# Kernel optimization log

Measured on AMD Instinct MI355X. Metric: run time of the kernel, lower is better.

Reference implementation:

```python
import jax, jax.numpy as jnp
import numpy as np

D_MODEL = 512
N_HEADS = 8
DEPTH = D_MODEL // N_HEADS
NEG_INF = -1000000000.0


def setup_inputs() -> dict:
    key = jax.random.key(0)
    ks = jax.random.split(key, 12)
    B, S = 4, 2048
    scale = 0.02
    return {
        "Q": jax.random.normal(ks[0], (B, S, D_MODEL), jnp.float32),
        "K": jax.random.normal(ks[1], (B, S, D_MODEL), jnp.float32),
        "V": jax.random.normal(ks[2], (B, S, D_MODEL), jnp.float32),
        "mask": jax.random.randint(ks[3], (B, S, S), 0, 2, jnp.int32),
        "Wq": jax.random.normal(ks[4], (D_MODEL, D_MODEL), jnp.float32) * scale,
        "bq": jnp.zeros((D_MODEL,), jnp.float32),
        "Wk": jax.random.normal(ks[5], (D_MODEL, D_MODEL), jnp.float32) * scale,
        "bk": jnp.zeros((D_MODEL,), jnp.float32),
        "Wv": jax.random.normal(ks[6], (D_MODEL, D_MODEL), jnp.float32) * scale,
        "bv": jnp.zeros((D_MODEL,), jnp.float32),
        "Wo": jax.random.normal(ks[7], (D_MODEL, D_MODEL), jnp.float32) * scale,
        "bo": jnp.zeros((D_MODEL,), jnp.float32),
    }


def _split_heads(x, B):
    # [B, S, d_model] -> [B, H, S, depth]
    S = x.shape[1]
    return x.reshape(B, S, N_HEADS, DEPTH).transpose(0, 2, 1, 3)


def reference(Q, K, V, mask, Wq, bq, Wk, bk, Wv, bv, Wo, bo):
    B, S, _ = Q.shape
    q = _split_heads(Q @ Wq + bq, B)  # [B,H,S,d]
    k = _split_heads(K @ Wk + bk, B)
    v = _split_heads(V @ Wv + bv, B)
    scores = jnp.einsum("bhqd,bhkd->bhqk", q, k) / jnp.sqrt(
        jnp.asarray(DEPTH, jnp.float32))
    m = mask[:, None, :, :]  # broadcast over heads: [B,1,S,S]
    scores = jnp.where(m == 0, jnp.asarray(NEG_INF, scores.dtype), scores)
    attn = jax.nn.softmax(scores, axis=-1)
    ctx = jnp.einsum("bhqk,bhkd->bhqd", attn, v)
    ctx = ctx.transpose(0, 2, 1, 3).reshape(B, S, D_MODEL)
    return ctx @ Wo + bo
```

## Files before the change

kernel.cpp:

```cpp
#include <hip/hip_runtime.h>
#include <hip/hip_bf16.h>
#include <stdint.h>

typedef unsigned short u16;
typedef unsigned int u32;
typedef unsigned long long u64;
using bf16x8 = __attribute__((ext_vector_type(8))) __bf16;
using f32x4  = __attribute__((ext_vector_type(4))) float;
using f32x16 = __attribute__((ext_vector_type(16))) float;

static constexpr int B_ = 4, H_ = 8, S_ = 2048, D_ = 64, DM_ = 512;
#define QSCALE 0.1803368801111601f

__device__ __forceinline__ u16 f2b(float f) {
  u32 u = __float_as_uint(f);
  u = (u + 0x7FFFu + ((u >> 16) & 1u)) >> 16;
  return (u16)u;
}

__device__ __forceinline__ u32 cvtpk_bf16(float a, float b) {
  u32 r;
  asm("v_cvt_pk_bf16_f32 %0, %1, %2" : "=v"(r) : "v"(a), "v"(b));
  return r;
}
__device__ __forceinline__ void plswap(u32& a, u32& b) {
  asm("v_permlane32_swap_b32 %0, %1" : "+v"(a), "+v"(b));
}
__device__ __forceinline__ void gload16(const void* g, void* lds) {
  __builtin_amdgcn_global_load_lds(
      (const __attribute__((address_space(1))) u32*)g,
      (__attribute__((address_space(3))) u32*)lds, 16, 0, 0);
}
#if __has_builtin(__builtin_amdgcn_exp2f)
__device__ __forceinline__ float exp2fast(float x) { return __builtin_amdgcn_exp2f(x); }
#else
__device__ __forceinline__ float exp2fast(float x) {
  float r;
  asm("v_exp_f32 %0, %1" : "=v"(r) : "v"(x));
  return r;
}
#endif
__device__ __forceinline__ float selmask(float ex, u64 pred) {
  float r;
  asm("v_cndmask_b32 %0, 0, %1, %2" : "=v"(r) : "v"(ex), "s"(pred));
  return r;
}

__global__ __launch_bounds__(256) void prep_w_kernel(
    const float* __restrict__ Wq, const float* __restrict__ Wk,
    const float* __restrict__ Wv, const float* __restrict__ Wo,
    u16* __restrict__ Wtq, u16* __restrict__ Wtk, u16* __restrict__ Wtv, u16* __restrict__ Wto) {
  __shared__ float tile[32][33];
  const int z = blockIdx.z;
  const float* W = z == 0 ? Wq : z == 1 ? Wk : z == 2 ? Wv : Wo;
  u16* Wt       = z == 0 ? Wtq : z == 1 ? Wtk : z == 2 ? Wtv : Wto;
  const int k0 = blockIdx.x * 32, n0 = blockIdx.y * 32;
  const int t = threadIdx.x;
  {
    const int kl = t >> 3, nl4 = (t & 7) * 4;
    float4 v = *(const float4*)(W + (size_t)(k0 + kl) * DM_ + n0 + nl4);
    tile[kl][nl4 + 0] = v.x; tile[kl][nl4 + 1] = v.y;
    tile[kl][nl4 + 2] = v.z; tile[kl][nl4 + 3] = v.w;
  }
  __syncthreads();
  {
    const int nl = t >> 3, kl4 = (t & 7) * 4;
    ushort4 o;
    o.x = f2b(tile[kl4 + 0][nl]); o.y = f2b(tile[kl4 + 1][nl]);
    o.z = f2b(tile[kl4 + 2][nl]); o.w = f2b(tile[kl4 + 3][nl]);
    *(ushort4*)(Wt + (size_t)(n0 + nl) * DM_ + k0 + kl4) = o;
  }
}

__global__ __launch_bounds__(256) void pack_mask_kernel(const int* __restrict__ mask,
                                                        u64* __restrict__ wmask) {
  __shared__ int mt[4][32][65];
  const int t = threadIdx.x, lane = t & 63, w = t >> 6;
  const int kt = blockIdx.x * 4 + w, qg = blockIdx.y, b = blockIdx.z;
  const int q0 = qg * 32;
  const int* src = mask + ((size_t)b * S_ + q0) * S_ + kt * 64 + lane;
#pragma unroll 8
  for (int i = 0; i < 32; ++i) mt[w][i][lane] = src[(size_t)i * S_];
  u64* dst = wmask + (((size_t)(b * 64 + qg) * 32 + kt) * 32);
  const int hi4 = (lane >> 5) * 4;
#pragma unroll
  for (int idx = 0; idx < 32; ++idx) {
    const int ksub = idx >> 4, r = idx & 15;
    const int key = ksub * 32 + (r & 3) + 8 * (r >> 2) + hi4;
    u64 bal = __ballot(mt[w][lane & 31][key] != 0);
    if (lane == 0) dst[idx] = bal;
  }
}

__global__ __launch_bounds__(256) void gemm_qkv_kernel(
    const float* __restrict__ Qf, const float* __restrict__ Kf, const float* __restrict__ Vf,
    const u16* __restrict__ Wtq, const u16* __restrict__ Wtk, const u16* __restrict__ Wtv,
    const float* __restrict__ bq, const float* __restrict__ bk, const float* __restrict__ bv,
    u16* __restrict__ qp, u16* __restrict__ kp, u16* __restrict__ vp) {
  __shared__ u16 As[128][40];
  __shared__ u16 Bs[128][40];
  const int z = blockIdx.z;
  const float* A    = z == 0 ? Qf : z == 1 ? Kf : Vf;
  const u16* Bt     = z == 0 ? Wtq : z == 1 ? Wtk : Wtv;
  const float* bias = z == 0 ? bq : z == 1 ? bk : bv;
  u16* outp         = z == 0 ? qp : z == 1 ? kp : vp;
  const float scale = z == 0 ? QSCALE : 1.0f;

  const int t = threadIdx.x;
  const int lane = t & 63, wid = t >> 6;
  const int wr = wid >> 1, wc = wid & 1;
  const int l15 = lane & 15, l4 = lane >> 4;
  const int cn = blockIdx.x * 128, rm = blockIdx.y * 128;
  const int srow = t >> 2, scol = (t & 3) << 3;

  f32x4 acc[4][4] = {};

  for (int k0 = 0; k0 < DM_; k0 += 32) {
    __syncthreads();
    {
      const float* a0 = A + (size_t)(rm + srow) * DM_ + k0 + scol;
      float4 f0 = *(const float4*)a0, f1 = *(const float4*)(a0 + 4);
      uint4 u;
      u.x = cvtpk_bf16(f0.x, f0.y); u.y = cvtpk_bf16(f0.z, f0.w);
      u.z = cvtpk_bf16(f1.x, f1.y); u.w = cvtpk_bf16(f1.z, f1.w);
      *(uint4*)(&As[srow][scol]) = u;
      const float* a1 = A + (size_t)(rm + srow + 64) * DM_ + k0 + scol;
      float4 g0 = *(const float4*)a1, g1 = *(const float4*)(a1 + 4);
      uint4 w2;
      w2.x = cvtpk_bf16(g0.x, g0.y); w2.y = cvtpk_bf16(g0.z, g0.w);
      w2.z = cvtpk_bf16(g1.x, g1.y); w2.w = cvtpk_bf16(g1.z, g1.w);
      *(uint4*)(&As[srow + 64][scol]) = w2;
    }
    *(uint4*)(&Bs[srow][scol])      = *(const uint4*)(Bt + (size_t)(cn + srow) * DM_ + k0 + scol);
    *(uint4*)(&Bs[srow + 64][scol]) = *(const uint4*)(Bt + (size_t)(cn + srow + 64) * DM_ + k0 + scol);
    __syncthreads();
    bf16x8 af[4], bfr[4];
#pragma unroll
    for (int m = 0; m < 4; ++m)
      af[m] = *(const bf16x8*)(&As[wr * 64 + m * 16 + l15][l4 * 8]);
#pragma unroll
    for (int n = 0; n < 4; ++n)
      bfr[n] = *(const bf16x8*)(&Bs[wc * 64 + n * 16 + l15][l4 * 8]);
#pragma unroll
    for (int m = 0; m < 4; ++m)
#pragma unroll
      for (int n = 0; n < 4; ++n)
        acc[m][n] = __builtin_amdgcn_mfma_f32_16x16x32_bf16(af[m], bfr[n], acc[m][n], 0, 0, 0);
  }

#pragma unroll
  for (int m = 0; m < 4; ++m)
#pragma unroll
    for (int n = 0; n < 4; ++n) {
      int col = cn + wc * 64 + n * 16 + l15;
      float bv_ = bias[col];
#pragma unroll
      for (int r = 0; r < 4; ++r) {
        int row = rm + wr * 64 + m * 16 + l4 * 4 + r;
        float v = (acc[m][n][r] + bv_) * scale;
        int b = row >> 11, s = row & 2047;
        int h = col >> 6, d = col & 63;
        if (z < 2)
          outp[(((size_t)(b * H_ + h)) * S_ + s) * D_ + d] = f2b(v);
        else
          outp[(((size_t)(b * H_ + h)) * D_ + d) * S_ + s] = f2b(v);
      }
    }
}

__global__ __launch_bounds__(256) void gemm_out_kernel(
    const u16* __restrict__ A, const u16* __restrict__ Bt,
    const float* __restrict__ bias, float* __restrict__ outp) {
  __shared__ u16 As[64][40];
  __shared__ u16 Bs[128][40];
  const int t = threadIdx.x;
  const int lane = t & 63, w = t >> 6;
  const int l15 = lane & 15, l4 = lane >> 4;
  const int cn = blockIdx.x * 128, rm = blockIdx.y * 64;
  const int srow = t >> 2, scol = (t & 3) << 3;

  f32x4 acc[4][2] = {};

  for (int k0 = 0; k0 < DM_; k0 += 32) {
    __syncthreads();
    *(uint4*)(&As[srow][scol])      = *(const uint4*)(A + (size_t)(rm + srow) * DM_ + k0 + scol);
    *(uint4*)(&Bs[srow][scol])      = *(const uint4*)(Bt + (size_t)(cn + srow) * DM_ + k0 + scol);
    *(uint4*)(&Bs[srow + 64][scol]) = *(const uint4*)(Bt + (size_t)(cn + srow + 64) * DM_ + k0 + scol);
    __syncthreads();
    bf16x8 af[4], bfr[2];
#pragma unroll
    for (int m = 0; m < 4; ++m)
      af[m] = *(const bf16x8*)(&As[m * 16 + l15][l4 * 8]);
#pragma unroll
    for (int n = 0; n < 2; ++n)
      bfr[n] = *(const bf16x8*)(&Bs[w * 32 + n * 16 + l15][l4 * 8]);
#pragma unroll
    for (int m = 0; m < 4; ++m)
#pragma unroll
      for (int n = 0; n < 2; ++n)
        acc[m][n] = __builtin_amdgcn_mfma_f32_16x16x32_bf16(af[m], bfr[n], acc[m][n], 0, 0, 0);
  }

#pragma unroll
  for (int m = 0; m < 4; ++m)
#pragma unroll
    for (int n = 0; n < 2; ++n) {
      int col = cn + w * 32 + n * 16 + l15;
      float bv_ = bias[col];
#pragma unroll
      for (int r = 0; r < 4; ++r) {
        int row = rm + m * 16 + l4 * 4 + r;
        outp[(size_t)row * DM_ + col] = acc[m][n][r] + bv_;
      }
    }
}

__global__ __launch_bounds__(256, 4) void attn_kernel(
    const u16* __restrict__ qp, const u16* __restrict__ kp, const u16* __restrict__ vp,
    const u64* __restrict__ wmask, u16* __restrict__ ctx) {
  __shared__ __align__(16) char smem[32768];
  const int t = threadIdx.x, lane = t & 63, w = t >> 6;
  const int l31 = lane & 31, hi = lane >> 5;
  const int ksub = w & 1, qsub = w >> 1;
  const int wu = __builtin_amdgcn_readfirstlane(w);
  const int wgid = blockIdx.x;
  const int h = wgid & 7, idx = wgid >> 3;
  const int b = idx >> 5, qt = idx & 31;
  const size_t head  = ((size_t)(b * H_ + h)) * S_ * D_;
  const size_t headT = ((size_t)(b * H_ + h)) * D_ * S_;
  const int q0 = qt * 64 + qsub * 32;
  const int q  = q0 + l31;

  bf16x8 qf[4];
  {
    const u16* qrow = qp + head + (size_t)q * D_;
#pragma unroll
    for (int ks = 0; ks < 4; ++ks) qf[ks] = *(const bf16x8*)(qrow + ks * 16 + hi * 8);
  }

  const u64* wm = wmask + (((size_t)(b * 64 + qt * 2 + (wu >> 1)) * 32) * 32) + (wu & 1) * 16;

  const int kxor = (l31 & 7) << 4;
  const int krbase = (ksub * 32 + l31) * 128;
  const int rbase0 = l31 * 128, rbase1 = (32 + l31) * 128;
  int colx[4];
#pragma unroll
  for (int s = 0; s < 4; ++s) colx[s] = ((s * 32 + hi * 16) ^ kxor);
  int vcolx[2];
#pragma unroll
  for (int s = 0; s < 2; ++s) vcolx[s] = ((ksub * 64 + s * 32 + hi * 16) ^ kxor);

  const int srow = lane >> 3;
  const int scol = ((lane & 7) ^ srow) << 3;
  const int c0 = w, c1 = w + 4;
  const u16* ksrc0 = kp + head + (size_t)(c0 * 8 + srow) * D_ + scol;
  const u16* ksrc1 = kp + head + (size_t)(c1 * 8 + srow) * D_ + scol;
  const u16* vsrc0 = vp + headT + (size_t)(c0 * 8 + srow) * S_ + scol;
  const u16* vsrc1 = vp + headT + (size_t)(c1 * 8 + srow) * S_ + scol;

  f32x16 accO0, accO1, lacc, FZ;
#pragma unroll
  for (int i = 0; i < 16; ++i) { accO0[i] = 0.f; accO1[i] = 0.f; lacc[i] = 0.f; FZ[i] = 0.f; }
  union { u32 wds[4]; bf16x8 v; } ones;
#pragma unroll
  for (int i = 0; i < 4; ++i) ones.wds[i] = 0x3F803F80u;

  auto stage = [&](int bufi, int kt) {
    char* kb = smem + bufi * 8192;
    char* vb = smem + 16384 + bufi * 8192;
    gload16(ksrc0 + (size_t)kt * 4096, kb + c0 * 1024);
    gload16(ksrc1 + (size_t)kt * 4096, kb + c1 * 1024);
    gload16(vsrc0 + kt * 64, vb + c0 * 1024);
    gload16(vsrc1 + kt * 64, vb + c1 * 1024);
  };

  stage(0, 0);
  u64 mskr[16];
#pragma unroll
  for (int r = 0; r < 16; ++r) mskr[r] = wm[r];
  __syncthreads();
  int buf = 0;

  for (int kt = 0; kt < S_ / 64; ++kt) {
    if (kt < S_ / 64 - 1) stage(buf ^ 1, kt + 1);

    const char* kb = smem + buf * 8192;
    const char* vb = smem + 16384 + buf * 8192;

    f32x16 s;
    {
      bf16x8 kf[4];
#pragma unroll
      for (int ks = 0; ks < 4; ++ks) kf[ks] = *(const bf16x8*)(kb + krbase + colx[ks]);
      __builtin_amdgcn_s_setprio(1);
      s = __builtin_amdgcn_mfma_f32_32x32x16_bf16(kf[0], qf[0], FZ, 0, 0, 0);
#pragma unroll
      for (int ks = 1; ks < 4; ++ks)
        s = __builtin_amdgcn_mfma_f32_32x32x16_bf16(kf[ks], qf[ks], s, 0, 0, 0);
      __builtin_amdgcn_s_setprio(0);
    }

    float e[16];
#pragma unroll
    for (int r = 0; r < 16; ++r) e[r] = selmask(exp2fast(s[r]), mskr[r]);

    {
      u32 pw[8];
#pragma unroll
      for (int j = 0; j < 8; ++j)
        pw[j] = cvtpk_bf16(e[2 * j], e[2 * j + 1]);
      plswap(pw[0], pw[2]); plswap(pw[1], pw[3]);
      plswap(pw[4], pw[6]); plswap(pw[5], pw[7]);
      __builtin_amdgcn_s_setprio(1);
#pragma unroll
      for (int s2 = 0; s2 < 2; ++s2) {
        union { u32 wds[4]; bf16x8 v; } pa;
        pa.wds[0] = pw[s2 * 4 + 0]; pa.wds[1] = pw[s2 * 4 + 1];
        pa.wds[2] = pw[s2 * 4 + 2]; pa.wds[3] = pw[s2 * 4 + 3];
        bf16x8 vf0 = *(const bf16x8*)(vb + rbase0 + vcolx[s2]);
        accO0 = __builtin_amdgcn_mfma_f32_32x32x16_bf16(pa.v, vf0, accO0, 0, 0, 0);
        bf16x8 vf1 = *(const bf16x8*)(vb + rbase1 + vcolx[s2]);
        accO1 = __builtin_amdgcn_mfma_f32_32x32x16_bf16(pa.v, vf1, accO1, 0, 0, 0);
        lacc = __builtin_amdgcn_mfma_f32_32x32x16_bf16(pa.v, ones.v, lacc, 0, 0, 0);
      }
      __builtin_amdgcn_s_setprio(0);
    }

    if (kt < S_ / 64 - 1) {
      const u64* wmk = wm + (kt + 1) * 32;
#pragma unroll
      for (int r = 0; r < 16; ++r) mskr[r] = wmk[r];
    }
    __syncthreads();
    buf ^= 1;
  }

  float (*Ol)[32][64] = (float (*)[32][64])smem;
  float (*La)[32] = (float (*)[32])(smem + 16384);
  if (ksub == 1) {
#pragma unroll
    for (int r = 0; r < 16; ++r) {
      const int qr = (r & 3) + 8 * (r >> 2) + 4 * hi;
      Ol[qsub][qr][l31]      = accO0[r];
      Ol[qsub][qr][32 + l31] = accO1[r];
      if (l31 == 0) La[qsub][qr] = lacc[r];
    }
  }
  __syncthreads();
  if (ksub == 0) {
    const int colA = h * 64 + l31, colB = h * 64 + 32 + l31;
#pragma unroll
    for (int r = 0; r < 16; ++r) {
      const int qr = (r & 3) + 8 * (r >> 2) + 4 * hi;
      const int row = q0 + qr;
      const float inv = 1.0f / (lacc[r] + La[qsub][qr]);
      u16* o = ctx + ((size_t)(b * S_) + row) * DM_;
      o[colA] = f2b((accO0[r] + Ol[qsub][qr][l31])      * inv);
      o[colB] = f2b((accO1[r] + Ol[qsub][qr][32 + l31]) * inv);
    }
  }
}

extern "C" void kernel_launch(void* const* d_in, const int* in_sizes, int n_in,
                              void* d_out, int out_size, void* d_ws, size_t ws_size,
                              hipStream_t stream) {
  const float* Q  = (const float*)d_in[0];
  const float* K  = (const float*)d_in[1];
  const float* V  = (const float*)d_in[2];
  const int* mask = (const int*)d_in[3];
  const float* Wq = (const float*)d_in[4];
  const float* bq = (const float*)d_in[5];
  const float* Wk = (const float*)d_in[6];
  const float* bk = (const float*)d_in[7];
  const float* Wv = (const float*)d_in[8];
  const float* bv = (const float*)d_in[9];
  const float* Wo = (const float*)d_in[10];
  const float* bo = (const float*)d_in[11];

  char* ws = (char*)d_ws;
  size_t off = 0;
  auto alloc = [&](size_t bytes) -> void* {
    void* p = ws + off;
    off += (bytes + 255) & ~(size_t)255;
    return p;
  };
  const size_t act_b = (size_t)B_ * S_ * DM_ * 2;
  u16* Wtq = (u16*)alloc((size_t)DM_ * DM_ * 2);
  u16* Wtk = (u16*)alloc((size_t)DM_ * DM_ * 2);
  u16* Wtv = (u16*)alloc((size_t)DM_ * DM_ * 2);
  u16* Wto = (u16*)alloc((size_t)DM_ * DM_ * 2);
  u64* wmask = (u64*)alloc((size_t)B_ * 64 * 32 * 32 * 8);
  u16* qp  = (u16*)alloc(act_b);
  u16* kp  = (u16*)alloc(act_b);
  u16* vp  = (u16*)alloc(act_b);
  u16* ctx = (u16*)alloc(act_b);

  prep_w_kernel<<<dim3(16, 16, 4), 256, 0, stream>>>(Wq, Wk, Wv, Wo, Wtq, Wtk, Wtv, Wto);
  pack_mask_kernel<<<dim3(8, 64, 4), 256, 0, stream>>>(mask, wmask);

  gemm_qkv_kernel<<<dim3(4, 64, 3), 256, 0, stream>>>(
      Q, K, V, Wtq, Wtk, Wtv, bq, bk, bv, qp, kp, vp);

  attn_kernel<<<dim3(1024), 256, 0, stream>>>(qp, kp, vp, wmask, ctx);

  gemm_out_kernel<<<dim3(4, 128), 256, 0, stream>>>(ctx, Wto, bo, (float*)d_out);
}
```

Baseline: 129.5 us.

## Pre-cast QKV inputs to bf16 and stage GEMM tiles via global_load_lds

Adds a separate kernel that converts the fp32 Q/K/V activations to bf16 once. Both GEMM kernels then load their tiles straight from global memory into LDS with global_load_lds, using an unpadded 64-byte-row layout. The aim is to cut register traffic and conversion work inside the GEMM loop. In exchange it adds an extra launch plus a full read and write of the activations, and the unpadded LDS rows may cause bank conflicts on the fragment reads.

```diff
diff --git a/kernel.cpp b/kernel.cpp
--- a/kernel.cpp
+++ b/kernel.cpp
@@ -44,6 +44,20 @@
   float r;
   asm("v_cndmask_b32 %0, 0, %1, %2" : "=v"(r) : "v"(ex), "s"(pred));
   return r;
+}
+
+__global__ __launch_bounds__(256) void cast3_kernel(
+    const float* __restrict__ Q, const float* __restrict__ K, const float* __restrict__ V,
+    u16* __restrict__ Qb, u16* __restrict__ Kb, u16* __restrict__ Vb) {
+  const int z = blockIdx.z;
+  const float* src = z == 0 ? Q : z == 1 ? K : V;
+  u16* dst        = z == 0 ? Qb : z == 1 ? Kb : Vb;
+  const int i = blockIdx.x * 256 + threadIdx.x;
+  float4 v = reinterpret_cast<const float4*>(src)[i];
+  uint2 o;
+  o.x = cvtpk_bf16(v.x, v.y);
+  o.y = cvtpk_bf16(v.z, v.w);
+  reinterpret_cast<uint2*>(dst)[i] = o;
 }
 
 __global__ __launch_bounds__(256) void prep_w_kernel(
@@ -93,14 +107,14 @@
 }
 
 __global__ __launch_bounds__(256) void gemm_qkv_kernel(
-    const float* __restrict__ Qf, const float* __restrict__ Kf, const float* __restrict__ Vf,
+    const u16* __restrict__ Qb, const u16* __restrict__ Kb, const u16* __restrict__ Vb,
     const u16* __restrict__ Wtq, const u16* __restrict__ Wtk, const u16* __restrict__ Wtv,
     const float* __restrict__ bq, const float* __restrict__ bk, const float* __restrict__ bv,
     u16* __restrict__ qp, u16* __restrict__ kp, u16* __restrict__ vp) {
-  __shared__ u16 As[128][40];
-  __shared__ u16 Bs[128][40];
+  __shared__ __align__(16) u16 As[128 * 32];
+  __shared__ __align__(16) u16 Bs[128 * 32];
   const int z = blockIdx.z;
-  const float* A    = z == 0 ? Qf : z == 1 ? Kf : Vf;
+  const u16* A      = z == 0 ? Qb : z == 1 ? Kb : Vb;
   const u16* Bt     = z == 0 ? Wtq : z == 1 ? Wtk : Wtv;
   const float* bias = z == 0 ? bq : z == 1 ? bk : bv;
   u16* outp         = z == 0 ? qp : z == 1 ? kp : vp;
@@ -111,36 +125,29 @@
   const int wr = wid >> 1, wc = wid & 1;
   const int l15 = lane & 15, l4 = lane >> 4;
   const int cn = blockIdx.x * 128, rm = blockIdx.y * 128;
-  const int srow = t >> 2, scol = (t & 3) << 3;
+
+  const int srow = wid * 16 + (lane >> 2), scol = (lane & 3) * 8;
+  const u16* asrc = A + (size_t)(rm + srow) * DM_ + scol;
+  const u16* bsrc = Bt + (size_t)(cn + srow) * DM_ + scol;
+  char* adst = (char*)As + wid * 1024;
+  char* bdst = (char*)Bs + wid * 1024;
 
   f32x4 acc[4][4] = {};
 
   for (int k0 = 0; k0 < DM_; k0 += 32) {
     __syncthreads();
-    {
-      const float* a0 = A + (size_t)(rm + srow) * DM_ + k0 + scol;
-      float4 f0 = *(const float4*)a0, f1 = *(const float4*)(a0 + 4);
-      uint4 u;
-      u.x = cvtpk_bf16(f0.x, f0.y); u.y = cvtpk_bf16(f0.z, f0.w);
-      u.z = cvtpk_bf16(f1.x, f1.y); u.w = cvtpk_bf16(f1.z, f1.w);
-      *(uint4*)(&As[srow][scol]) = u;
-      const float* a1 = A + (size_t)(rm + srow + 64) * DM_ + k0 + scol;
-      float4 g0 = *(const float4*)a1, g1 = *(const float4*)(a1 + 4);
-      uint4 w2;
-      w2.x = cvtpk_bf16(g0.x, g0.y); w2.y = cvtpk_bf16(g0.z, g0.w);
-      w2.z = cvtpk_bf16(g1.x, g1.y); w2.w = cvtpk_bf16(g1.z, g1.w);
-      *(uint4*)(&As[srow + 64][scol]) = w2;
-    }
-    *(uint4*)(&Bs[srow][scol])      = *(const uint4*)(Bt + (size_t)(cn + srow) * DM_ + k0 + scol);
-    *(uint4*)(&Bs[srow + 64][scol]) = *(const uint4*)(Bt + (size_t)(cn + srow + 64) * DM_ + k0 + scol);
+    gload16(asrc + k0, adst);
+    gload16(asrc + (size_t)64 * DM_ + k0, adst + 4096);
+    gload16(bsrc + k0, bdst);
+    gload16(bsrc + (size_t)64 * DM_ + k0, bdst + 4096);
     __syncthreads();
     bf16x8 af[4], bfr[4];
 #pragma unroll
     for (int m = 0; m < 4; ++m)
-      af[m] = *(const bf16x8*)(&As[wr * 64 + m * 16 + l15][l4 * 8]);
+      af[m] = *(const bf16x8*)((const char*)As + (wr * 64 + m * 16 + l15) * 64 + l4 * 16);
 #pragma unroll
     for (int n = 0; n < 4; ++n)
-      bfr[n] = *(const bf16x8*)(&Bs[wc * 64 + n * 16 + l15][l4 * 8]);
+      bfr[n] = *(const bf16x8*)((const char*)Bs + (wc * 64 + n * 16 + l15) * 64 + l4 * 16);
 #pragma unroll
     for (int m = 0; m < 4; ++m)
 #pragma unroll
@@ -171,29 +178,34 @@
 __global__ __launch_bounds__(256) void gemm_out_kernel(
     const u16* __restrict__ A, const u16* __restrict__ Bt,
     const float* __restrict__ bias, float* __restrict__ outp) {
-  __shared__ u16 As[64][40];
-  __shared__ u16 Bs[128][40];
+  __shared__ __align__(16) u16 As[64 * 32];
+  __shared__ __align__(16) u16 Bs[128 * 32];
   const int t = threadIdx.x;
   const int lane = t & 63, w = t >> 6;
   const int l15 = lane & 15, l4 = lane >> 4;
   const int cn = blockIdx.x * 128, rm = blockIdx.y * 64;
-  const int srow = t >> 2, scol = (t & 3) << 3;
+
+  const int srow = w * 16 + (lane >> 2), scol = (lane & 3) * 8;
+  const u16* asrc = A + (size_t)(rm + srow) * DM_ + scol;
+  const u16* bsrc = Bt + (size_t)(cn + srow) * DM_ + scol;
+  char* adst = (char*)As + w * 1024;
+  char* bdst = (char*)Bs + w * 1024;
 
   f32x4 acc[4][2] = {};
 
   for (int k0 = 0; k0 < DM_; k0 += 32) {
     __syncthreads();
-    *(uint4*)(&As[srow][scol])      = *(const uint4*)(A + (size_t)(rm + srow) * DM_ + k0 + scol);
-    *(uint4*)(&Bs[srow][scol])      = *(const uint4*)(Bt + (size_t)(cn + srow) * DM_ + k0 + scol);
-    *(uint4*)(&Bs[srow + 64][scol]) = *(const uint4*)(Bt + (size_t)(cn + srow + 64) * DM_ + k0 + scol);
+    gload16(asrc + k0, adst);
+    gload16(bsrc + k0, bdst);
+    gload16(bsrc + (size_t)64 * DM_ + k0, bdst + 4096);
     __syncthreads();
     bf16x8 af[4], bfr[2];
 #pragma unroll
     for (int m = 0; m < 4; ++m)
-      af[m] = *(const bf16x8*)(&As[m * 16 + l15][l4 * 8]);
+      af[m] = *(const bf16x8*)((const char*)As + (m * 16 + l15) * 64 + l4 * 16);
 #pragma unroll
     for (int n = 0; n < 2; ++n)
-      bfr[n] = *(const bf16x8*)(&Bs[w * 32 + n * 16 + l15][l4 * 8]);
+      bfr[n] = *(const bf16x8*)((const char*)Bs + (w * 32 + n * 16 + l15) * 64 + l4 * 16);
 #pragma unroll
     for (int m = 0; m < 4; ++m)
 #pragma unroll
@@ -390,6 +402,9 @@
   u16* Wtv = (u16*)alloc((size_t)DM_ * DM_ * 2);
   u16* Wto = (u16*)alloc((size_t)DM_ * DM_ * 2);
   u64* wmask = (u64*)alloc((size_t)B_ * 64 * 32 * 32 * 8);
+  u16* Qb  = (u16*)alloc(act_b);
+  u16* Kb  = (u16*)alloc(act_b);
+  u16* Vb  = (u16*)alloc(act_b);
   u16* qp  = (u16*)alloc(act_b);
   u16* kp  = (u16*)alloc(act_b);
   u16* vp  = (u16*)alloc(act_b);
@@ -397,9 +412,10 @@
 
   prep_w_kernel<<<dim3(16, 16, 4), 256, 0, stream>>>(Wq, Wk, Wv, Wo, Wtq, Wtk, Wtv, Wto);
   pack_mask_kernel<<<dim3(8, 64, 4), 256, 0, stream>>>(mask, wmask);
+  cast3_kernel<<<dim3((B_ * S_ * DM_ / 4) / 256, 1, 3), 256, 0, stream>>>(Q, K, V, Qb, Kb, Vb);
 
   gemm_qkv_kernel<<<dim3(4, 64, 3), 256, 0, stream>>>(
-      Q, K, V, Wtq, Wtk, Wtv, bq, bk, bv, qp, kp, vp);
+      Qb, Kb, Vb, Wtq, Wtk, Wtv, bq, bk, bv, qp, kp, vp);
 
   attn_kernel<<<dim3(1024), 256, 0, stream>>>(qp, kp, vp, wmask, ctx);
 
```

New measurement: 130.6 us. Within noise of the previous version (+0.9%).

## Double-buffer projection GEMMs with direct global-to-LDS async loads

Applied to the files above, without the earlier changes.

Both projection GEMM kernels now stage tiles into double-buffered shared memory through a gload16 helper, which appears to be a direct global-to-LDS load. The next k-tile is fetched while the current one feeds the MFMAs, and there is one barrier per iteration instead of two. In the QKV kernel the fp32 activations are kept as fp32 in LDS and converted to bf16 at fragment-read time, which doubles LDS footprint and read traffic for A. The unpadded LDS layout may add bank conflicts, and correctness depends on gload16 completing before the barrier.

```diff
diff --git a/kernel.cpp b/kernel.cpp
--- a/kernel.cpp
+++ b/kernel.cpp
@@ -97,8 +97,8 @@
     const u16* __restrict__ Wtq, const u16* __restrict__ Wtk, const u16* __restrict__ Wtv,
     const float* __restrict__ bq, const float* __restrict__ bk, const float* __restrict__ bv,
     u16* __restrict__ qp, u16* __restrict__ kp, u16* __restrict__ vp) {
-  __shared__ u16 As[128][40];
-  __shared__ u16 Bs[128][40];
+  __shared__ __align__(16) float As[2][128 * 32];
+  __shared__ __align__(16) u16  Bs[2][128 * 32];
   const int z = blockIdx.z;
   const float* A    = z == 0 ? Qf : z == 1 ? Kf : Vf;
   const u16* Bt     = z == 0 ? Wtq : z == 1 ? Wtk : Wtv;
@@ -111,41 +111,50 @@
   const int wr = wid >> 1, wc = wid & 1;
   const int l15 = lane & 15, l4 = lane >> 4;
   const int cn = blockIdx.x * 128, rm = blockIdx.y * 128;
-  const int srow = t >> 2, scol = (t & 3) << 3;
+
+  const int arow = t >> 3, acol = (t & 7) * 4;
+  const float* asrc = A + (size_t)(rm + arow) * DM_ + acol;
+  const int brow = t >> 2, bcol = (t & 3) * 8;
+  const u16* bsrc = Bt + (size_t)(cn + brow) * DM_ + bcol;
+
+  auto stage = [&](int bufi, int k0) {
+    char* adst = (char*)As[bufi] + wid * 1024;
+    char* bdst = (char*)Bs[bufi] + wid * 1024;
+#pragma unroll
+    for (int i = 0; i < 4; ++i)
+      gload16(asrc + (size_t)(i * 32) * DM_ + k0, adst + i * 4096);
+    gload16(bsrc + k0, bdst);
+    gload16(bsrc + (size_t)64 * DM_ + k0, bdst + 4096);
+  };
 
   f32x4 acc[4][4] = {};
 
+  stage(0, 0);
+  __syncthreads();
+  int buf = 0;
+
   for (int k0 = 0; k0 < DM_; k0 += 32) {
-    __syncthreads();
-    {
-      const float* a0 = A + (size_t)(rm + srow) * DM_ + k0 + scol;
-      float4 f0 = *(const float4*)a0, f1 = *(const float4*)(a0 + 4);
-      uint4 u;
-      u.x = cvtpk_bf16(f0.x, f0.y); u.y = cvtpk_bf16(f0.z, f0.w);
-      u.z = cvtpk_bf16(f1.x, f1.y); u.w = cvtpk_bf16(f1.z, f1.w);
-      *(uint4*)(&As[srow][scol]) = u;
-      const float* a1 = A + (size_t)(rm + srow + 64) * DM_ + k0 + scol;
-      float4 g0 = *(const float4*)a1, g1 = *(const float4*)(a1 + 4);
-      uint4 w2;
-      w2.x = cvtpk_bf16(g0.x, g0.y); w2.y = cvtpk_bf16(g0.z, g0.w);
-      w2.z = cvtpk_bf16(g1.x, g1.y); w2.w = cvtpk_bf16(g1.z, g1.w);
-      *(uint4*)(&As[srow + 64][scol]) = w2;
-    }
-    *(uint4*)(&Bs[srow][scol])      = *(const uint4*)(Bt + (size_t)(cn + srow) * DM_ + k0 + scol);
-    *(uint4*)(&Bs[srow + 64][scol]) = *(const uint4*)(Bt + (size_t)(cn + srow + 64) * DM_ + k0 + scol);
-    __syncthreads();
+    if (k0 + 32 < DM_) stage(buf ^ 1, k0 + 32);
     bf16x8 af[4], bfr[4];
 #pragma unroll
-    for (int m = 0; m < 4; ++m)
-      af[m] = *(const bf16x8*)(&As[wr * 64 + m * 16 + l15][l4 * 8]);
+    for (int m = 0; m < 4; ++m) {
+      const float* ap = As[buf] + (wr * 64 + m * 16 + l15) * 32 + l4 * 8;
+      float4 x = *(const float4*)ap, y = *(const float4*)(ap + 4);
+      union { u32 wds[4]; bf16x8 v; } c;
+      c.wds[0] = cvtpk_bf16(x.x, x.y); c.wds[1] = cvtpk_bf16(x.z, x.w);
+      c.wds[2] = cvtpk_bf16(y.x, y.y); c.wds[3] = cvtpk_bf16(y.z, y.w);
+      af[m] = c.v;
+    }
 #pragma unroll
     for (int n = 0; n < 4; ++n)
-      bfr[n] = *(const bf16x8*)(&Bs[wc * 64 + n * 16 + l15][l4 * 8]);
+      bfr[n] = *(const bf16x8*)((const char*)Bs[buf] + (wc * 64 + n * 16 + l15) * 64 + l4 * 16);
 #pragma unroll
     for (int m = 0; m < 4; ++m)
 #pragma unroll
       for (int n = 0; n < 4; ++n)
         acc[m][n] = __builtin_amdgcn_mfma_f32_16x16x32_bf16(af[m], bfr[n], acc[m][n], 0, 0, 0);
+    __syncthreads();
+    buf ^= 1;
   }
 
 #pragma unroll
@@ -171,34 +180,45 @@
 __global__ __launch_bounds__(256) void gemm_out_kernel(
     const u16* __restrict__ A, const u16* __restrict__ Bt,
     const float* __restrict__ bias, float* __restrict__ outp) {
-  __shared__ u16 As[64][40];
-  __shared__ u16 Bs[128][40];
+  __shared__ __align__(16) u16 As[2][64 * 32];
+  __shared__ __align__(16) u16 Bs[2][128 * 32];
   const int t = threadIdx.x;
   const int lane = t & 63, w = t >> 6;
   const int l15 = lane & 15, l4 = lane >> 4;
   const int cn = blockIdx.x * 128, rm = blockIdx.y * 64;
-  const int srow = t >> 2, scol = (t & 3) << 3;
+
+  const int srow = w * 16 + (lane >> 2), scol = (lane & 3) * 8;
+  const u16* asrc = A + (size_t)(rm + srow) * DM_ + scol;
+  const u16* bsrc = Bt + (size_t)(cn + srow) * DM_ + scol;
+
+  auto stage = [&](int bufi, int k0) {
+    gload16(asrc + k0, (char*)As[bufi] + w * 1024);
+    gload16(bsrc + k0, (char*)Bs[bufi] + w * 1024);
+    gload16(bsrc + (size_t)64 * DM_ + k0, (char*)Bs[bufi] + w * 1024 + 4096);
+  };
 
   f32x4 acc[4][2] = {};
 
+  stage(0, 0);
+  __syncthreads();
+  int buf = 0;
+
   for (int k0 = 0; k0 < DM_; k0 += 32) {
-    __syncthreads();
-    *(uint4*)(&As[srow][scol])      = *(const uint4*)(A + (size_t)(rm + srow) * DM_ + k0 + scol);
-    *(uint4*)(&Bs[srow][scol])      = *(const uint4*)(Bt + (size_t)(cn + srow) * DM_ + k0 + scol);
-    *(uint4*)(&Bs[srow + 64][scol]) = *(const uint4*)(Bt + (size_t)(cn + srow + 64) * DM_ + k0 + scol);
-    __syncthreads();
+    if (k0 + 32 < DM_) stage(buf ^ 1, k0 + 32);
     bf16x8 af[4], bfr[2];
 #pragma unroll
     for (int m = 0; m < 4; ++m)
-      af[m] = *(const bf16x8*)(&As[m * 16 + l15][l4 * 8]);
+      af[m] = *(const bf16x8*)((const char*)As[buf] + (m * 16 + l15) * 64 + l4 * 16);
 #pragma unroll
     for (int n = 0; n < 2; ++n)
-      bfr[n] = *(const bf16x8*)(&Bs[w * 32 + n * 16 + l15][l4 * 8]);
+      bfr[n] = *(const bf16x8*)((const char*)Bs[buf] + (w * 32 + n * 16 + l15) * 64 + l4 * 16);
 #pragma unroll
     for (int m = 0; m < 4; ++m)
 #pragma unroll
       for (int n = 0; n < 2; ++n)
         acc[m][n] = __builtin_amdgcn_mfma_f32_16x16x32_bf16(af[m], bfr[n], acc[m][n], 0, 0, 0);
+    __syncthreads();
+    buf ^= 1;
   }
 
 #pragma unroll
```

New measurement: 130.3 us. No clear change (+0.6%).
